# Kernel optimization log

Measured on AMD Instinct MI355X. Metric: run time of the kernel, lower is better.

Reference implementation:

```python
import jax, jax.numpy as jnp
import numpy as np

B, S, E = 2, 2048, 2048
H = 16              # num value heads
D = E // H // 2     # = 64, half head dim (Q/K head dim)
LAMBDA_INIT = 0.8 - 0.6 * float(np.exp(-0.3 * 12))
NORM_EPS = 1e-5


def setup_inputs() -> dict:
    key = jax.random.key(0)
    ks = jax.random.split(key, 10)
    std = 0.02
    x = jax.random.normal(ks[0], (B, S, E), jnp.float32)
    Wq = jax.random.normal(ks[1], (E, E), jnp.float32) * std
    Wk = jax.random.normal(ks[2], (E, E), jnp.float32) * std
    Wv = jax.random.normal(ks[3], (E, E), jnp.float32) * std
    Wo = jax.random.normal(ks[4], (E, E), jnp.float32) * std
    lambda_q1 = jax.random.normal(ks[5], (D,), jnp.float32) * 0.1
    lambda_q2 = jax.random.normal(ks[6], (D,), jnp.float32) * 0.1
    lambda_k1 = jax.random.normal(ks[7], (D,), jnp.float32) * 0.1
    lambda_k2 = jax.random.normal(ks[8], (D,), jnp.float32) * 0.1
    norm_w = jnp.ones((2 * D,), jnp.float32)
    # standard RoPE angle table: (S, D//2)
    inv_freq = 1.0 / (10000.0 ** (np.arange(0, D, 2, dtype=np.float32) / D))
    ang = np.outer(np.arange(S, dtype=np.float32), inv_freq)
    freqs_cos = jnp.asarray(np.cos(ang), jnp.float32)
    freqs_sin = jnp.asarray(np.sin(ang), jnp.float32)
    return {"x": x, "Wq": Wq, "Wk": Wk, "Wv": Wv, "Wo": Wo,
            "lambda_q1": lambda_q1, "lambda_q2": lambda_q2,
            "lambda_k1": lambda_k1, "lambda_k2": lambda_k2,
            "norm_w": norm_w, "freqs_cos": freqs_cos, "freqs_sin": freqs_sin,
            "start_pos": 0}


def _rope(t, cos, sin):
    # t: (B, S, nh, D); complex rotation over pairs along last dim
    tr = t.reshape(*t.shape[:-1], -1, 2)
    tre, tim = tr[..., 0], tr[..., 1]
    c = cos[None, :, None, :]
    s = sin[None, :, None, :]
    out_re = tre * c - tim * s
    out_im = tre * s + tim * c
    return jnp.stack([out_re, out_im], axis=-1).reshape(t.shape)


def reference(x, Wq, Wk, Wv, Wo, lambda_q1, lambda_q2, lambda_k1, lambda_k2,
              norm_w, freqs_cos, freqs_sin, start_pos):
    bsz, tgt_len, _ = x.shape
    scaling = D ** (-0.5)
    q = (x @ Wq.T).reshape(bsz, tgt_len, 2 * H, D)
    k = (x @ Wk.T).reshape(bsz, tgt_len, 2 * H, D)
    v = (x @ Wv.T).reshape(bsz, tgt_len, H, 2 * D)
    q = _rope(q, freqs_cos, freqs_sin)
    k = _rope(k, freqs_cos, freqs_sin)
    q = (q * scaling).transpose(0, 2, 1, 3)      # (B, 2H, S, D)
    keys = k.transpose(0, 2, 1, 3)               # (B, 2H, S, D)
    values = v.transpose(0, 2, 1, 3)             # (B, H, S, 2D)
    scores = jnp.einsum('bhsd,bhtd->bhst', q, keys)
    causal = jnp.where(jnp.arange(tgt_len)[None, :] > jnp.arange(tgt_len)[:, None],
                       jnp.float32(-jnp.inf), jnp.float32(0.0))
    scores = scores + causal
    attn = jax.nn.softmax(scores.astype(jnp.float32), axis=-1)
    lam1 = jnp.exp(jnp.sum(lambda_q1 * lambda_k1))
    lam2 = jnp.exp(jnp.sum(lambda_q2 * lambda_k2))
    lambda_full = lam1 - lam2 + LAMBDA_INIT
    attn = attn.reshape(bsz, H, 2, tgt_len, tgt_len)
    attn_diff = attn[:, :, 0] - lambda_full * attn[:, :, 1]   # (B, H, S, S)
    ctx = jnp.einsum('bhst,bhtd->bhsd', attn_diff, values)    # (B, H, S, 2D)
    # per-head RMSNorm over 2D channel dim
    ctx = ctx * jax.lax.rsqrt(jnp.mean(ctx * ctx, axis=-1, keepdims=True) + NORM_EPS)
    ctx = ctx * norm_w
    ctx = ctx.transpose(0, 2, 1, 3).reshape(bsz, tgt_len, H * 2 * D)
    return ctx @ Wo.T
```

## Files before the change

### kernel.cpp

```cpp
#include <hip/hip_runtime.h>
#include <hip/hip_bf16.h>
#include <stdint.h>

typedef __hip_bfloat16 bf16;
typedef __attribute__((ext_vector_type(8))) short short8;
typedef __attribute__((ext_vector_type(4))) float floatx4;

#define MFMA16(a, b, c) __builtin_amdgcn_mfma_f32_16x16x32_bf16((a), (b), (c), 0, 0, 0)
#define LAMBDA_INIT_F 0.7836057665f

__device__ __forceinline__ void async16(const void* g, void* l) {
    __builtin_amdgcn_global_load_lds(
        (const __attribute__((address_space(1))) void*)g,
        (__attribute__((address_space(3))) void*)(uintptr_t)l,
        16, 0, 0);
}

__device__ __forceinline__ float loadf(const void* p, size_t idx, int isbf) {
    if (isbf) return __bfloat162float(((const bf16*)p)[idx]);
    return ((const float*)p)[idx];
}

__global__ void detect_dtype(const unsigned short* __restrict__ x, int* __restrict__ flag) {
    const int t = threadIdx.x;
    const unsigned short u = x[2 * t];
    const int e = (u >> 7) & 0xFF;
    int sane = (e >= 110 && e <= 130) ? 1 : 0;
#pragma unroll
    for (int m = 32; m > 0; m >>= 1) sane += __shfl_xor(sane, m);
    if (t == 0) flag[0] = (sane >= 32) ? 1 : 0;
}

__global__ __launch_bounds__(256) void to_bf16(const void* __restrict__ src,
                                               bf16* __restrict__ dst, int n,
                                               const int* __restrict__ flag) {
    const int i = (blockIdx.x * 256 + threadIdx.x) * 8;
    if (i >= n) return;
    if (flag[0]) {
        *(short8*)(dst + i) = *(const short8*)((const bf16*)src + i);
    } else {
        const float* f = (const float*)src + i;
        short8 r;
#pragma unroll
        for (int j = 0; j < 8; ++j) {
            bf16 h = __float2bfloat16(f[j]);
            r[j] = __builtin_bit_cast(short, h);
        }
        *(short8*)(dst + i) = r;
    }
}

__global__ __launch_bounds__(256) void gemm_bt_bf(const bf16* __restrict__ A,
                                                  const bf16* __restrict__ B,
                                                  void* __restrict__ C,
                                                  int M, int N, int K,
                                                  const int* __restrict__ flag, int c_raw) {
    __shared__ __align__(16) bf16 As[128 * 32];
    __shared__ __align__(16) bf16 Bs[128 * 32];
    const int c_bf = c_raw ? flag[0] : 1;

    const int tid  = threadIdx.x;
    const int lane = tid & 63;
    const int quad = lane >> 4;
    const int l16  = lane & 15;
    const int w    = tid >> 6;
    const int wr   = w >> 1, wc = w & 1;
    const int bm   = blockIdx.y, bn = blockIdx.x;

    floatx4 acc[4][4];
#pragma unroll
    for (int i = 0; i < 4; ++i)
#pragma unroll
        for (int j = 0; j < 4; ++j)
#pragma unroll
            for (int r = 0; r < 4; ++r) acc[i][j][r] = 0.0f;

    for (int k0 = 0; k0 < K; k0 += 32) {
        __syncthreads();
#pragma unroll
        for (int i = 0; i < 2; ++i) {
            const int c     = i * 256 + tid;
            const int row   = c >> 2;
            const int inner = c & 3;
            async16(A + (size_t)(bm * 128 + row) * K + k0 + inner * 8, (char*)As + c * 16);
            async16(B + (size_t)(bn * 128 + row) * K + k0 + inner * 8, (char*)Bs + c * 16);
        }
        __syncthreads();

        short8 af[4], bfr[4];
#pragma unroll
        for (int i = 0; i < 4; ++i)
            af[i] = *(const short8*)((const char*)As + (wr * 64 + i * 16 + l16) * 64 + quad * 16);
#pragma unroll
        for (int j = 0; j < 4; ++j)
            bfr[j] = *(const short8*)((const char*)Bs + (wc * 64 + j * 16 + l16) * 64 + quad * 16);
#pragma unroll
        for (int i = 0; i < 4; ++i)
#pragma unroll
            for (int j = 0; j < 4; ++j)
                acc[i][j] = MFMA16(af[i], bfr[j], acc[i][j]);
    }

#pragma unroll
    for (int i = 0; i < 4; ++i)
#pragma unroll
        for (int j = 0; j < 4; ++j) {
            const int n = bn * 128 + wc * 64 + j * 16 + l16;
#pragma unroll
            for (int r = 0; r < 4; ++r) {
                const int m = bm * 128 + wr * 64 + i * 16 + quad * 4 + r;
                if (c_bf) ((bf16*)C)[(size_t)m * N + n] = __float2bfloat16(acc[i][j][r]);
                else      ((float*)C)[(size_t)m * N + n] = acc[i][j][r];
            }
        }
}

__global__ __launch_bounds__(256) void rope_scale(bf16* __restrict__ q, bf16* __restrict__ k,
                                                  const void* __restrict__ fcos,
                                                  const void* __restrict__ fsin,
                                                  const int* __restrict__ flag) {
    const int isbf = flag[0];
    const int p = blockIdx.x * 256 + threadIdx.x;
    const int j = p & 31;
    const int s = (p >> 10) & 2047;
    const float c  = loadf(fcos, s * 32 + j, isbf);
    const float sn = loadf(fsin, s * 32 + j, isbf);

    __hip_bfloat162* q2 = (__hip_bfloat162*)q;
    __hip_bfloat162* k2 = (__hip_bfloat162*)k;

    __hip_bfloat162 qv = q2[p];
    float re = __bfloat162float(qv.x), im = __bfloat162float(qv.y);
    __hip_bfloat162 o;
    o.x = __float2bfloat16((re * c - im * sn) * 0.125f);
    o.y = __float2bfloat16((re * sn + im * c) * 0.125f);
    q2[p] = o;

    __hip_bfloat162 kv = k2[p];
    re = __bfloat162float(kv.x); im = __bfloat162float(kv.y);
    o.x = __float2bfloat16(re * c - im * sn);
    o.y = __float2bfloat16(re * sn + im * c);
    k2[p] = o;
}

__global__ __launch_bounds__(256) void transpose_v(const bf16* __restrict__ V,
                                                   bf16* __restrict__ Vt) {
    __shared__ bf16 tile[32][33];
    const int sb = blockIdx.x * 32;
    const int db = blockIdx.y * 32;
    const int bh = blockIdx.z;
    const int c  = threadIdx.x & 31;
    const int ty = threadIdx.x >> 5;
#pragma unroll
    for (int i = 0; i < 4; ++i) {
        const int r = ty + i * 8;
        tile[r][c] = V[((size_t)((bh >> 4) * 2048 + sb + r) * 16 + (bh & 15)) * 128 + db + c];
    }
    __syncthreads();
#pragma unroll
    for (int i = 0; i < 4; ++i) {
        const int r = ty + i * 8;
        Vt[((size_t)bh * 128 + db + r) * 2048 + sb + c] = tile[c][r];
    }
}

__global__ void lambda_kernel(const void* lq1, const void* lq2,
                              const void* lk1, const void* lk2,
                              float* out, const int* __restrict__ flag) {
    const int isbf = flag[0];
    const int t = threadIdx.x;
    float p1 = loadf(lq1, t, isbf) * loadf(lk1, t, isbf);
    float p2 = loadf(lq2, t, isbf) * loadf(lk2, t, isbf);
#pragma unroll
    for (int m = 32; m > 0; m >>= 1) {
        p1 += __shfl_xor(p1, m);
        p2 += __shfl_xor(p2, m);
    }
    if (t == 0) out[0] = expf(p1) - expf(p2) + LAMBDA_INIT_F;
}

__global__ __launch_bounds__(256) void diff_attn(const bf16* __restrict__ Q,
                                                 const bf16* __restrict__ K,
                                                 const bf16* __restrict__ Vt,
                                                 bf16* __restrict__ ctx,
                                                 const float* __restrict__ lam,
                                                 const void* __restrict__ norm_w,
                                                 const int* __restrict__ flag) {
    __shared__ __align__(16) char smem[55296];
    bf16* K1s = (bf16*)smem;
    bf16* K2s = (bf16*)(smem + 8192);
    bf16* Vs  = (bf16*)(smem + 16384);
    char* pool = smem + 32768;

    const int isbf = flag[0];
    const int tid  = threadIdx.x;
    const int lane = tid & 63;
    const int quad = lane >> 4;
    const int l16  = lane & 15;
    const int w    = tid >> 6;
    const int t7   = l16 & 7;

    const int bidx = blockIdx.x;
    const int p  = bidx & 15;
    const int h  = (bidx >> 4) & 15;
    const int b  = bidx >> 8;

    const float lambda_full = lam[0];
    float nw[8];
#pragma unroll
    for (int j = 0; j < 8; ++j) nw[j] = loadf(norm_w, j * 16 + l16, isbf);

    bf16* P1s = (bf16*)(pool + w * 2816);
    bf16* P2s = (bf16*)(pool + 11264 + w * 2816);

    for (int tsel = 0; tsel < 2; ++tsel) {
        const int qt = tsel ? (31 - p) : p;
        const int q0 = qt * 64;

        __syncthreads();

#pragma unroll
        for (int i = 0; i < 2; ++i) {
            const int c = i * 256 + tid;
            const int row = c >> 3, cc = c & 7;
            const int inner = cc ^ (row & 7);
            async16(Q + ((size_t)(b * 2048 + q0 + row) * 32 + 2 * h) * 64 + inner * 8,
                    pool + c * 16);
            async16(Q + ((size_t)(b * 2048 + q0 + row) * 32 + 2 * h + 1) * 64 + inner * 8,
                    pool + 8192 + c * 16);
        }
        __syncthreads();

        short8 qf1[2], qf2[2];
        {
            const int rho = w * 16 + l16;
#pragma unroll
            for (int c = 0; c < 2; ++c) {
                const int ch = (c * 4 + quad) ^ t7;
                qf1[c] = *(const short8*)(pool + rho * 128 + ch * 16);
                qf2[c] = *(const short8*)(pool + 8192 + rho * 128 + ch * 16);
            }
        }

        floatx4 O1[8], O2[8];
#pragma unroll
        for (int j = 0; j < 8; ++j)
#pragma unroll
            for (int r = 0; r < 4; ++r) { O1[j][r] = 0.0f; O2[j][r] = 0.0f; }
        float lp1[4] = {0.f, 0.f, 0.f, 0.f};
        float lp2[4] = {0.f, 0.f, 0.f, 0.f};

        for (int kt0 = 0; kt0 <= q0; kt0 += 64) {
            __syncthreads();
#pragma unroll
            for (int i = 0; i < 2; ++i) {
                const int c = i * 256 + tid;
                const int row = c >> 3, cc = c & 7;
                const int inner = cc ^ (row & 7);
                async16(K + ((size_t)(b * 2048 + kt0 + row) * 32 + 2 * h) * 64 + inner * 8,
                        (char*)K1s + c * 16);
                async16(K + ((size_t)(b * 2048 + kt0 + row) * 32 + 2 * h + 1) * 64 + inner * 8,
                        (char*)K2s + c * 16);
            }
#pragma unroll
            for (int i = 0; i < 4; ++i) {
                const int c = i * 256 + tid;
                const int d = c >> 3, cc = c & 7;
                const int inner = cc ^ (d & 7);
                async16(Vt + ((size_t)(b * 16 + h) * 128 + d) * 2048 + kt0 + inner * 8,
                        (char*)Vs + c * 16);
            }
            __syncthreads();

            floatx4 s1[4], s2[4];
#pragma unroll
            for (int j = 0; j < 4; ++j)
#pragma unroll
                for (int r = 0; r < 4; ++r) { s1[j][r] = 0.0f; s2[j][r] = 0.0f; }
#pragma unroll
            for (int c = 0; c < 2; ++c) {
                const int ch = ((c * 4 + quad) ^ t7) * 16;
#pragma unroll
                for (int j = 0; j < 4; ++j) {
                    short8 k1f = *(const short8*)((const char*)K1s + (j * 16 + l16) * 128 + ch);
                    s1[j] = MFMA16(qf1[c], k1f, s1[j]);
                    short8 k2f = *(const short8*)((const char*)K2s + (j * 16 + l16) * 128 + ch);
                    s2[j] = MFMA16(qf2[c], k2f, s2[j]);
                }
            }

            if (kt0 == q0) {
#pragma unroll
                for (int j = 0; j < 4; ++j)
#pragma unroll
                    for (int r = 0; r < 4; ++r)
                        if (j * 16 + l16 > w * 16 + quad * 4 + r) {
                            s1[j][r] = -1e30f;
                            s2[j][r] = -1e30f;
                        }
            }

#pragma unroll
            for (int j = 0; j < 4; ++j)
#pragma unroll
                for (int r = 0; r < 4; ++r) {
                    const float e1 = __expf(s1[j][r]);
                    const float e2 = __expf(s2[j][r]);
                    lp1[r] += e1;
                    lp2[r] += e2;
                    P1s[(quad * 4 + r) * 88 + j * 16 + l16] = __float2bfloat16(e1);
                    P2s[(quad * 4 + r) * 88 + j * 16 + l16] = __float2bfloat16(e2);
                }

#pragma unroll
            for (int c = 0; c < 2; ++c) {
                short8 a1 = *(const short8*)((const char*)P1s + l16 * 176 + c * 64 + quad * 16);
                short8 a2 = *(const short8*)((const char*)P2s + l16 * 176 + c * 64 + quad * 16);
                const int ch = ((c * 4 + quad) ^ t7) * 16;
#pragma unroll
                for (int j = 0; j < 8; ++j) {
                    short8 vb = *(const short8*)((const char*)Vs + (j * 16 + l16) * 128 + ch);
                    O1[j] = MFMA16(a1, vb, O1[j]);
                    O2[j] = MFMA16(a2, vb, O2[j]);
                }
            }
        }

#pragma unroll
        for (int r = 0; r < 4; ++r) {
            float t1 = lp1[r], t2 = lp2[r];
            t1 += __shfl_xor(t1, 1); t2 += __shfl_xor(t2, 1);
            t1 += __shfl_xor(t1, 2); t2 += __shfl_xor(t2, 2);
            t1 += __shfl_xor(t1, 4); t2 += __shfl_xor(t2, 4);
            t1 += __shfl_xor(t1, 8); t2 += __shfl_xor(t2, 8);
            const float i1 = 1.0f / t1;
            const float i2 = lambda_full / t2;
            float cv[8];
            float ss = 0.0f;
#pragma unroll
            for (int j = 0; j < 8; ++j) {
                const float v = O1[j][r] * i1 - O2[j][r] * i2;
                cv[j] = v;
                ss += v * v;
            }
            ss += __shfl_xor(ss, 1);
            ss += __shfl_xor(ss, 2);
            ss += __shfl_xor(ss, 4);
            ss += __shfl_xor(ss, 8);
            const float scale = rsqrtf(ss * (1.0f / 128.0f) + 1e-5f);
            const int row = q0 + w * 16 + quad * 4 + r;
            const size_t base = ((size_t)(b * 2048) + row) * 2048 + h * 128;
#pragma unroll
            for (int j = 0; j < 8; ++j)
                ctx[base + j * 16 + l16] = __float2bfloat16(cv[j] * scale * nw[j]);
        }
    }
}

extern "C" void kernel_launch(void* const* d_in, const int* in_sizes, int n_in,
                              void* d_out, int out_size, void* d_ws, size_t ws_size,
                              hipStream_t stream) {
    const void* x   = d_in[0];
    const void* Wq  = d_in[1];
    const void* Wk  = d_in[2];
    const void* Wv  = d_in[3];
    const void* Wo  = d_in[4];
    const void* lq1 = d_in[5];
    const void* lq2 = d_in[6];
    const void* lk1 = d_in[7];
    const void* lk2 = d_in[8];
    const void* nw  = d_in[9];
    const void* fc  = d_in[10];
    const void* fs  = d_in[11];

    const size_t BUF = (size_t)4096 * 2048 * sizeof(bf16);
    if (ws_size < 4 * BUF + 64) return;
    char* ws = (char*)d_ws;
    bf16*  qbuf  = (bf16*)(ws);
    bf16*  kbuf  = (bf16*)(ws + BUF);
    bf16*  vbuf  = (bf16*)(ws + 2 * BUF);
    bf16*  vtbuf = (bf16*)(ws + 3 * BUF);
    float* lamb  = (float*)(ws + 4 * BUF);
    int*   flag  = (int*)(ws + 4 * BUF + 8);
    bf16*  xb    = vtbuf;
    bf16*  wslot = (bf16*)d_out;
    bf16*  ctxb  = vbuf;

    const int NX = 2 * 2048 * 2048;
    const int NW = 2048 * 2048;

    detect_dtype<<<1, 64, 0, stream>>>((const unsigned short*)x, flag);
    to_bf16<<<NX / 2048, 256, 0, stream>>>(x, xb, NX, flag);

    dim3 gg(16, 32);
    to_bf16<<<NW / 2048, 256, 0, stream>>>(Wq, wslot, NW, flag);
    gemm_bt_bf<<<gg, 256, 0, stream>>>(xb, wslot, qbuf, 4096, 2048, 2048, flag, 0);
    to_bf16<<<NW / 2048, 256, 0, stream>>>(Wk, wslot, NW, flag);
    gemm_bt_bf<<<gg, 256, 0, stream>>>(xb, wslot, kbuf, 4096, 2048, 2048, flag, 0);
    to_bf16<<<NW / 2048, 256, 0, stream>>>(Wv, wslot, NW, flag);
    gemm_bt_bf<<<gg, 256, 0, stream>>>(xb, wslot, vbuf, 4096, 2048, 2048, flag, 0);

    rope_scale<<<16384, 256, 0, stream>>>(qbuf, kbuf, fc, fs, flag);
    transpose_v<<<dim3(64, 4, 32), 256, 0, stream>>>(vbuf, vtbuf);
    lambda_kernel<<<1, 64, 0, stream>>>(lq1, lq2, lk1, lk2, lamb, flag);

    diff_attn<<<512, 256, 0, stream>>>(qbuf, kbuf, vtbuf, ctxb, lamb, nw, flag);

    to_bf16<<<NW / 2048, 256, 0, stream>>>(Wo, qbuf, NW, flag);
    gemm_bt_bf<<<gg, 256, 0, stream>>>(ctxb, qbuf, d_out, 4096, 2048, 2048, flag, 1);
}
```

Before: 555.9 us.

## Fuse RoPE and V transpose into projection GEMM epilogues, remap attention blocks

The Q and K projection GEMMs now apply RoPE (and the 1/8 query scale) in their epilogue, exchanging each rotation pair between lanes with a shuffle. The V GEMM writes its output already transposed per head, so the separate rope_scale and transpose_v kernels and their extra passes over Q, K and V are gone. The attention kernel's block-index mapping is also reordered to interleave heads, which may change scheduling and cache locality. The cost is per-element cos/sin loads in the GEMM epilogue and narrow strided 8-byte stores for the transposed V.

```diff
diff --git a/kernel.cpp b/kernel.cpp
--- a/kernel.cpp
+++ b/kernel.cpp
@@ -4,6 +4,7 @@
 
 typedef __hip_bfloat16 bf16;
 typedef __attribute__((ext_vector_type(8))) short short8;
+typedef __attribute__((ext_vector_type(4))) short s4v;
 typedef __attribute__((ext_vector_type(4))) float floatx4;
 
 #define MFMA16(a, b, c) __builtin_amdgcn_mfma_f32_16x16x32_bf16((a), (b), (c), 0, 0, 0)
@@ -50,14 +51,16 @@
     }
 }
 
-__global__ __launch_bounds__(256) void gemm_bt_bf(const bf16* __restrict__ A,
+__global__ __launch_bounds__(256) void gemm_bt_ep(const bf16* __restrict__ A,
                                                   const bf16* __restrict__ B,
                                                   void* __restrict__ C,
                                                   int M, int N, int K,
-                                                  const int* __restrict__ flag, int c_raw) {
+                                                  const int* __restrict__ flag,
+                                                  const void* __restrict__ fcos,
+                                                  const void* __restrict__ fsin,
+                                                  int mode) {
     __shared__ __align__(16) bf16 As[128 * 32];
     __shared__ __align__(16) bf16 Bs[128 * 32];
-    const int c_bf = c_raw ? flag[0] : 1;
 
     const int tid  = threadIdx.x;
     const int lane = tid & 63;
@@ -101,66 +104,59 @@
                 acc[i][j] = MFMA16(af[i], bfr[j], acc[i][j]);
     }
 
-#pragma unroll
-    for (int i = 0; i < 4; ++i)
-#pragma unroll
-        for (int j = 0; j < 4; ++j) {
-            const int n = bn * 128 + wc * 64 + j * 16 + l16;
-#pragma unroll
-            for (int r = 0; r < 4; ++r) {
-                const int m = bm * 128 + wr * 64 + i * 16 + quad * 4 + r;
-                if (c_bf) ((bf16*)C)[(size_t)m * N + n] = __float2bfloat16(acc[i][j][r]);
-                else      ((float*)C)[(size_t)m * N + n] = acc[i][j][r];
-            }
-        }
-}
-
-__global__ __launch_bounds__(256) void rope_scale(bf16* __restrict__ q, bf16* __restrict__ k,
-                                                  const void* __restrict__ fcos,
-                                                  const void* __restrict__ fsin,
-                                                  const int* __restrict__ flag) {
     const int isbf = flag[0];
-    const int p = blockIdx.x * 256 + threadIdx.x;
-    const int j = p & 31;
-    const int s = (p >> 10) & 2047;
-    const float c  = loadf(fcos, s * 32 + j, isbf);
-    const float sn = loadf(fsin, s * 32 + j, isbf);
-
-    __hip_bfloat162* q2 = (__hip_bfloat162*)q;
-    __hip_bfloat162* k2 = (__hip_bfloat162*)k;
-
-    __hip_bfloat162 qv = q2[p];
-    float re = __bfloat162float(qv.x), im = __bfloat162float(qv.y);
-    __hip_bfloat162 o;
-    o.x = __float2bfloat16((re * c - im * sn) * 0.125f);
-    o.y = __float2bfloat16((re * sn + im * c) * 0.125f);
-    q2[p] = o;
-
-    __hip_bfloat162 kv = k2[p];
-    re = __bfloat162float(kv.x); im = __bfloat162float(kv.y);
-    o.x = __float2bfloat16(re * c - im * sn);
-    o.y = __float2bfloat16(re * sn + im * c);
-    k2[p] = o;
-}
-
-__global__ __launch_bounds__(256) void transpose_v(const bf16* __restrict__ V,
-                                                   bf16* __restrict__ Vt) {
-    __shared__ bf16 tile[32][33];
-    const int sb = blockIdx.x * 32;
-    const int db = blockIdx.y * 32;
-    const int bh = blockIdx.z;
-    const int c  = threadIdx.x & 31;
-    const int ty = threadIdx.x >> 5;
-#pragma unroll
-    for (int i = 0; i < 4; ++i) {
-        const int r = ty + i * 8;
-        tile[r][c] = V[((size_t)((bh >> 4) * 2048 + sb + r) * 16 + (bh & 15)) * 128 + db + c];
-    }
-    __syncthreads();
-#pragma unroll
-    for (int i = 0; i < 4; ++i) {
-        const int r = ty + i * 8;
-        Vt[((size_t)bh * 128 + db + r) * 2048 + sb + c] = tile[c][r];
+    if (mode == 3) {
+#pragma unroll
+        for (int i = 0; i < 4; ++i)
+#pragma unroll
+            for (int j = 0; j < 4; ++j) {
+                const int n  = bn * 128 + wc * 64 + j * 16 + l16;
+                const int m0 = bm * 128 + wr * 64 + i * 16 + quad * 4;
+                const int bb = m0 >> 11;
+                const int s0 = m0 & 2047;
+                s4v pk;
+#pragma unroll
+                for (int r = 0; r < 4; ++r) {
+                    bf16 hv = __float2bfloat16(acc[i][j][r]);
+                    pk[r] = __builtin_bit_cast(short, hv);
+                }
+                *(s4v*)((bf16*)C + ((size_t)(bb * 2048 + n)) * 2048 + s0) = pk;
+            }
+    } else if (mode == 1 || mode == 2) {
+        const float qs = (mode == 1) ? 0.125f : 1.0f;
+#pragma unroll
+        for (int i = 0; i < 4; ++i)
+#pragma unroll
+            for (int j = 0; j < 4; ++j) {
+                const int n   = bn * 128 + wc * 64 + j * 16 + l16;
+                const int jp  = (n & 63) >> 1;
+                const float sg = (n & 1) ? 1.0f : -1.0f;
+#pragma unroll
+                for (int r = 0; r < 4; ++r) {
+                    const int m = bm * 128 + wr * 64 + i * 16 + quad * 4 + r;
+                    const int s = m & 2047;
+                    const float v  = acc[i][j][r];
+                    const float pv = __shfl_xor(v, 1);
+                    const float ct = loadf(fcos, (size_t)s * 32 + jp, isbf);
+                    const float st = loadf(fsin, (size_t)s * 32 + jp, isbf);
+                    const float out = (v * ct + sg * pv * st) * qs;
+                    ((bf16*)C)[(size_t)m * N + n] = __float2bfloat16(out);
+                }
+            }
+    } else {
+        const int c_bf = (mode == 4) ? isbf : 1;
+#pragma unroll
+        for (int i = 0; i < 4; ++i)
+#pragma unroll
+            for (int j = 0; j < 4; ++j) {
+                const int n = bn * 128 + wc * 64 + j * 16 + l16;
+#pragma unroll
+                for (int r = 0; r < 4; ++r) {
+                    const int m = bm * 128 + wr * 64 + i * 16 + quad * 4 + r;
+                    if (c_bf) ((bf16*)C)[(size_t)m * N + n] = __float2bfloat16(acc[i][j][r]);
+                    else      ((float*)C)[(size_t)m * N + n] = acc[i][j][r];
+                }
+            }
     }
 }
 
@@ -201,9 +197,12 @@
     const int t7   = l16 & 7;
 
     const int bidx = blockIdx.x;
-    const int p  = bidx & 15;
-    const int h  = (bidx >> 4) & 15;
-    const int b  = bidx >> 8;
+    const int c8   = bidx & 7;
+    const int r6   = bidx >> 3;
+    const int p    = r6 & 15;
+    const int grp  = (r6 >> 4) * 8 + c8;
+    const int h    = grp & 15;
+    const int b    = grp >> 4;
 
     const float lambda_full = lam[0];
     float nw[8];
@@ -382,7 +381,7 @@
     bf16*  vtbuf = (bf16*)(ws + 3 * BUF);
     float* lamb  = (float*)(ws + 4 * BUF);
     int*   flag  = (int*)(ws + 4 * BUF + 8);
-    bf16*  xb    = vtbuf;
+    bf16*  xb    = vbuf;
     bf16*  wslot = (bf16*)d_out;
     bf16*  ctxb  = vbuf;
 
@@ -394,18 +393,16 @@
 
     dim3 gg(16, 32);
     to_bf16<<<NW / 2048, 256, 0, stream>>>(Wq, wslot, NW, flag);
-    gemm_bt_bf<<<gg, 256, 0, stream>>>(xb, wslot, qbuf, 4096, 2048, 2048, flag, 0);
+    gemm_bt_ep<<<gg, 256, 0, stream>>>(xb, wslot, qbuf, 4096, 2048, 2048, flag, fc, fs, 1);
     to_bf16<<<NW / 2048, 256, 0, stream>>>(Wk, wslot, NW, flag);
-    gemm_bt_bf<<<gg, 256, 0, stream>>>(xb, wslot, kbuf, 4096, 2048, 2048, flag, 0);
+    gemm_bt_ep<<<gg, 256, 0, stream>>>(xb, wslot, kbuf, 4096, 2048, 2048, flag, fc, fs, 2);
     to_bf16<<<NW / 2048, 256, 0, stream>>>(Wv, wslot, NW, flag);
-    gemm_bt_bf<<<gg, 256, 0, stream>>>(xb, wslot, vbuf, 4096, 2048, 2048, flag, 0);
-
-    rope_scale<<<16384, 256, 0, stream>>>(qbuf, kbuf, fc, fs, flag);
-    transpose_v<<<dim3(64, 4, 32), 256, 0, stream>>>(vbuf, vtbuf);
+    gemm_bt_ep<<<gg, 256, 0, stream>>>(xb, wslot, vtbuf, 4096, 2048, 2048, flag, fc, fs, 3);
+
     lambda_kernel<<<1, 64, 0, stream>>>(lq1, lq2, lk1, lk2, lamb, flag);
 
     diff_attn<<<512, 256, 0, stream>>>(qbuf, kbuf, vtbuf, ctxb, lamb, nw, flag);
 
     to_bf16<<<NW / 2048, 256, 0, stream>>>(Wo, qbuf, NW, flag);
-    gemm_bt_bf<<<gg, 256, 0, stream>>>(ctxb, qbuf, d_out, 4096, 2048, 2048, flag, 1);
-}
+    gemm_bt_ep<<<gg, 256, 0, stream>>>(ctxb, qbuf, d_out, 4096, 2048, 2048, flag, fc, fs, 4);
+}
```

After: 542.1 us. -2.5%, faster.
